# Optimization experiments

Measured on AMD Instinct MI355X. Metric: run time of the kernel, lower is better.

Reference implementation:

```python
import jax, jax.numpy as jnp
import numpy as np

B, N_HEADS, DIM, HS, WS = 8, 8, 256, 64, 64
CH = DIM // N_HEADS          # 32 head dim
HIDDEN = max(DIM // 2, 32)   # 128 SE hidden (r=2)
SCALE = CH ** -0.5
# CoaT-style CRPE: window sizes 3,5,7 over head groups (2,3,3)

def _dwconv(x, w, b):
    # depthwise conv, x: [B, Cg, H, W], w: [Cg, 1, kw, kw]
    y = jax.lax.conv_general_dilated(
        x, w, (1, 1), 'SAME',
        dimension_numbers=('NCHW', 'OIHW', 'NCHW'),
        feature_group_count=x.shape[1])
    return y + b[None, :, None, None]

def setup_inputs() -> dict:
    key = jax.random.key(0)
    ks = jax.random.split(key, 8)
    s = 0.02
    return {
        'x': jax.random.normal(ks[0], (B, HS * WS, DIM), jnp.float32),
        'qkv_w': jax.random.normal(ks[1], (3 * DIM, DIM), jnp.float32) * s,
        'qkv_b': jnp.zeros((3 * DIM,), jnp.float32),
        'proj_w': jax.random.normal(ks[2], (DIM, DIM), jnp.float32) * s,
        'proj_b': jnp.zeros((DIM,), jnp.float32),
        'se_w1': jax.random.normal(ks[3], (HIDDEN, DIM), jnp.float32) * s,
        'se_w2': jax.random.normal(ks[4], (N_HEADS, HIDDEN), jnp.float32) * s,
        'crpe_w3': jax.random.normal(ks[5], (2 * CH, 1, 3, 3), jnp.float32) * s,
        'crpe_b3': jnp.zeros((2 * CH,), jnp.float32),
        'crpe_w5': jax.random.normal(ks[6], (3 * CH, 1, 5, 5), jnp.float32) * s,
        'crpe_b5': jnp.zeros((3 * CH,), jnp.float32),
        'crpe_w7': jax.random.normal(ks[7], (3 * CH, 1, 7, 7), jnp.float32) * s,
        'crpe_b7': jnp.zeros((3 * CH,), jnp.float32),
        'H': HS, 'W': WS,
    }

def _crpe(q, v, H, W, w3, b3, w5, b5, w7, b7):
    # q, v: [B, h, N, Ch]; N == H*W
    Bq, h, N, Ch = q.shape
    v_img = v.transpose(0, 1, 3, 2).reshape(Bq, h * Ch, H, W)
    c0, c1 = 2 * Ch, 5 * Ch  # head splits (2,3,3)
    y = jnp.concatenate([
        _dwconv(v_img[:, :c0], w3, b3),
        _dwconv(v_img[:, c0:c1], w5, b5),
        _dwconv(v_img[:, c1:], w7, b7),
    ], axis=1)
    conv_v = y.reshape(Bq, h, Ch, N).transpose(0, 1, 3, 2)
    return q * conv_v  # Hadamard rel-pos term

def reference(x, qkv_w, qkv_b, proj_w, proj_b, se_w1, se_w2,
              crpe_w3, crpe_b3, crpe_w5, crpe_b5, crpe_w7, crpe_b7, H, W):
    Bx, N, C = x.shape
    qkv = (x @ qkv_w.T + qkv_b).reshape(Bx, N, 3, N_HEADS, CH)
    qkv = qkv.transpose(2, 0, 3, 1, 4)  # [3, B, h, N, Ch]
    q, k, v = qkv[0], qkv[1], qkv[2]
    crpe = _crpe(q, v, H, W, crpe_w3, crpe_b3, crpe_w5, crpe_b5, crpe_w7, crpe_b7)
    k_softmax = jax.nn.softmax(k, axis=2)  # softmax over tokens N
    ktv = jnp.einsum('bhnk,bhnv->bhkv', k_softmax, v)     # [B,h,Ch,Ch]
    factor_att = jnp.einsum('bhnk,bhkv->bhnv', q, ktv)    # [B,h,N,Ch]
    factor_att = SCALE * factor_att + crpe
    # SE-style domain gating: mean-pool over N -> conv1x1 -> relu -> conv1x1 -> sigmoid
    pooled = factor_att.mean(axis=2).reshape(Bx, N_HEADS * CH)  # [B, C]
    hid = jax.nn.relu(pooled @ se_w1.T)                         # [B, HIDDEN]
    gate = jax.nn.sigmoid(hid @ se_w2.T)                        # [B, h]
    out = factor_att * (1.0 + gate[:, :, None, None])           # gate*fa + fa
    out = out.transpose(0, 2, 1, 3).reshape(Bx, N, C)
    return out @ proj_w.T + proj_b
```

## Files before the change

kernel.cpp:

```cpp
#include <hip/hip_runtime.h>

namespace {

constexpr float kScale = 0.17677669529663687f;

typedef __attribute__((ext_vector_type(8))) short bf16x8;
typedef __attribute__((ext_vector_type(4))) short bf16x4;
typedef __attribute__((ext_vector_type(4))) float f32x4;

__device__ __forceinline__ short bf_hi(float x) {
  unsigned u = __float_as_uint(x);
  return (short)((u + 0x7FFFu + ((u >> 16) & 1u)) >> 16);
}
__device__ __forceinline__ short bf_lo(float x) {
  unsigned u = __float_as_uint(x);
  unsigned hi = (u + 0x7FFFu + ((u >> 16) & 1u)) & 0xFFFF0000u;
  float r = x - __uint_as_float(hi);
  unsigned u2 = __float_as_uint(r);
  return (short)((u2 + 0x7FFFu + ((u2 >> 16) & 1u)) >> 16);
}

__device__ __forceinline__ bf16x8 cvt8v(const float4 f0, const float4 f1,
                                        bool lo) {
  bf16x8 v;
  if (lo) {
    v[0] = bf_lo(f0.x); v[1] = bf_lo(f0.y); v[2] = bf_lo(f0.z);
    v[3] = bf_lo(f0.w); v[4] = bf_lo(f1.x); v[5] = bf_lo(f1.y);
    v[6] = bf_lo(f1.z); v[7] = bf_lo(f1.w);
  } else {
    v[0] = bf_hi(f0.x); v[1] = bf_hi(f0.y); v[2] = bf_hi(f0.z);
    v[3] = bf_hi(f0.w); v[4] = bf_hi(f1.x); v[5] = bf_hi(f1.y);
    v[6] = bf_hi(f1.z); v[7] = bf_hi(f1.w);
  }
  return v;
}

__global__ __launch_bounds__(1024) void wsplit2_kernel(
    const float* __restrict__ w, short* __restrict__ wsplit2) {
  const int nc = blockIdx.x;
  const int ct = nc / 24, j = nc % 24;
  const int r = j >> 3, kc = j & 7;
  const bool lo = (r == 1);
  const int u = threadIdx.x;
  const int col = u >> 2, kq = u & 3;
  const float* src = &w[(size_t)(ct * 256 + col) * 256 + kc * 32 + kq * 8];
  const float4 f0 = *reinterpret_cast<const float4*>(src);
  const float4 f1 = *reinterpret_cast<const float4*>(src + 4);
  *reinterpret_cast<bf16x8*>(&wsplit2[(size_t)nc * 8192 + u * 8]) =
      cvt8v(f0, f1, lo);
}

__global__ __launch_bounds__(1024) void pwsplit_kernel(
    const float* __restrict__ w, short* __restrict__ pw) {
  const int nc = blockIdx.x;
  const int r = nc >> 3, kc = nc & 7;
  const bool lo = (r == 1);
  const int u = threadIdx.x;
  const int col = u >> 2, kq = u & 3;
  const float* src = &w[(size_t)col * 256 + kc * 32 + kq * 8];
  const float4 f0 = *reinterpret_cast<const float4*>(src);
  const float4 f1 = *reinterpret_cast<const float4*>(src + 4);
  *reinterpret_cast<bf16x8*>(&pw[(size_t)nc * 8192 + u * 8]) =
      cvt8v(f0, f1, lo);
}

__global__ __launch_bounds__(512, 1) void qkv_mfma_kernel(
    const float* __restrict__ x, const short* __restrict__ wsplit2,
    const float* __restrict__ bias, float* __restrict__ q,
    float* __restrict__ kk, float* __restrict__ v) {
  __shared__ short As[128][520];
  __shared__ short Bs[256][40];
  const int tid = threadIdx.x;
  const int row0 = blockIdx.x * 128;
  const int wave = tid >> 6, lane = tid & 63;
  const int wr = (wave >> 2) * 64;
  const int wc = (wave & 3) * 64;
  const int l15 = lane & 15, l4 = lane >> 4;

  bf16x8 brgA[2], brgB[2];
  auto bload = [&](int nc, bf16x8 (&brg)[2]) {
    const short* src = wsplit2 + (size_t)nc * 8192;
#pragma unroll
    for (int i = 0; i < 2; ++i)
      brg[i] = *reinterpret_cast<const bf16x8*>(src + (tid + i * 512) * 8);
  };
  bload(0, brgA);
  bload(1, brgB);

#pragma unroll 4
  for (int i = 0; i < 16; ++i) {
    const int f = tid + i * 512;
    const int r = f >> 6, c = (f & 63) * 4;
    const float4 a4 = *reinterpret_cast<const float4*>(
        &x[(size_t)(row0 + r) * 256 + c]);
    bf16x4 h, l;
    h[0] = bf_hi(a4.x); h[1] = bf_hi(a4.y); h[2] = bf_hi(a4.z);
    h[3] = bf_hi(a4.w);
    l[0] = bf_lo(a4.x); l[1] = bf_lo(a4.y); l[2] = bf_lo(a4.z);
    l[3] = bf_lo(a4.w);
    *reinterpret_cast<bf16x4*>(&As[r][c]) = h;
    *reinterpret_cast<bf16x4*>(&As[r][256 + c]) = l;
  }
  __syncthreads();

  f32x4 acc[4][4];
  auto step = [&](int nc, bf16x8 (&brg)[2]) {
#pragma unroll
    for (int i = 0; i < 2; ++i) {
      const int u = tid + i * 512;
      *reinterpret_cast<bf16x8*>(&Bs[u >> 2][(u & 3) * 8]) = brg[i];
    }
    __syncthreads();
    if (nc + 2 < 72) bload(nc + 2, brg);
    const int j = nc % 24;
    const int r = j >> 3, kc = j & 7;
    const int aoff = (r == 2 ? 256 : 0) + kc * 32;
    bf16x8 af[4], bfr[4];
#pragma unroll
    for (int f = 0; f < 4; ++f) {
      af[f] = *reinterpret_cast<const bf16x8*>(
          &As[wr + f * 16 + l15][aoff + l4 * 8]);
      bfr[f] = *reinterpret_cast<const bf16x8*>(&Bs[wc + f * 16 + l15][l4 * 8]);
    }
#pragma unroll
    for (int fi = 0; fi < 4; ++fi)
#pragma unroll
      for (int fj = 0; fj < 4; ++fj)
        acc[fi][fj] = __builtin_amdgcn_mfma_f32_16x16x32_bf16(
            af[fi], bfr[fj], acc[fi][fj], 0, 0, 0);
    __syncthreads();
  };

  for (int ct = 0; ct < 3; ++ct) {
#pragma unroll
    for (int i = 0; i < 4; ++i)
#pragma unroll
      for (int j = 0; j < 4; ++j) acc[i][j] = (f32x4){0.f, 0.f, 0.f, 0.f};

    for (int j2 = 0; j2 < 12; ++j2) {
      step(ct * 24 + j2 * 2, brgA);
      step(ct * 24 + j2 * 2 + 1, brgB);
    }
    float* dst = (ct == 0) ? q : (ct == 1) ? kk : v;
#pragma unroll
    for (int fj = 0; fj < 4; ++fj) {
      const int col = wc + fj * 16 + l15;
      const int hh = col >> 5, cc = col & 31;
      const float bv = bias[ct * 256 + col];
#pragma unroll
      for (int fi = 0; fi < 4; ++fi) {
#pragma unroll
        for (int jj = 0; jj < 4; ++jj) {
          const int rr = row0 + wr + fi * 16 + l4 * 4 + jj;
          const int bb = rr >> 12, n = rr & 4095;
          dst[((size_t)(bb * 8 + hh) * 4096 + n) * 32 + cc] =
              acc[fi][fj][jj] + bv;
        }
      }
    }
  }
}

__global__ __launch_bounds__(256) void ktv_partial_kernel(
    const float* __restrict__ k, const float* __restrict__ v,
    float* __restrict__ pev, float* __restrict__ pe) {
  const int bh = blockIdx.x;
  const int chunk = blockIdx.y;
  const float* kb = k + (size_t)bh * 131072 + (size_t)chunk * 256 * 32;
  const float* vb = v + (size_t)bh * 131072 + (size_t)chunk * 256 * 32;
  __shared__ __align__(16) float ks[32][32];
  __shared__ __align__(16) float vs[32][32];
  const int t = threadIdx.x;
  const int kc = t >> 3;
  const int vg = (t & 7) * 4;
  const int sr = t >> 3, sc = (t & 7) * 4;
  float a0 = 0.f, a1 = 0.f, a2 = 0.f, a3 = 0.f, se = 0.f;
  for (int n0 = 0; n0 < 256; n0 += 32) {
    __syncthreads();
    const float4 k4 =
        *reinterpret_cast<const float4*>(&kb[(size_t)(n0 + sr) * 32 + sc]);
    const float4 v4 =
        *reinterpret_cast<const float4*>(&vb[(size_t)(n0 + sr) * 32 + sc]);
    *reinterpret_cast<float4*>(&ks[sr][sc]) = k4;
    *reinterpret_cast<float4*>(&vs[sr][sc]) = v4;
    __syncthreads();
#pragma unroll
    for (int r = 0; r < 32; ++r) {
      const float e = __expf(ks[r][kc]);
      se += e;
      const float4 vv = *reinterpret_cast<const float4*>(&vs[r][vg]);
      a0 = fmaf(e, vv.x, a0); a1 = fmaf(e, vv.y, a1);
      a2 = fmaf(e, vv.z, a2); a3 = fmaf(e, vv.w, a3);
    }
  }
  float* o = pev + ((size_t)(bh * 16 + chunk)) * 1024 + kc * 32 + vg;
  o[0] = a0; o[1] = a1; o[2] = a2; o[3] = a3;
  if ((t & 7) == 0) pe[(bh * 16 + chunk) * 32 + kc] = se;
}

__global__ __launch_bounds__(256) void ktv_reduce_kernel(
    const float* __restrict__ pev, const float* __restrict__ pe,
    float* __restrict__ ktv) {
  const int bh = blockIdx.x;
  const int t = threadIdx.x;
  const int kc = t >> 3, vg = (t & 7) * 4;
  float a0 = 0.f, a1 = 0.f, a2 = 0.f, a3 = 0.f, se = 0.f;
  for (int ch = 0; ch < 16; ++ch) {
    const float4 p4 = *reinterpret_cast<const float4*>(
        &pev[((size_t)(bh * 16 + ch)) * 1024 + kc * 32 + vg]);
    a0 += p4.x; a1 += p4.y; a2 += p4.z; a3 += p4.w;
    se += pe[(bh * 16 + ch) * 32 + kc];
  }
  const float inv = 1.0f / se;
  float* o = ktv + (size_t)bh * 1024 + kc * 32 + vg;
  o[0] = a0 * inv; o[1] = a1 * inv; o[2] = a2 * inv; o[3] = a3 * inv;
}

template <int K>
__device__ __forceinline__ void crpe_tile(const float (*lds)[64][32],
                                          const float* __restrict__ wch,
                                          float bias, int c, int x0,
                                          float* __restrict__ outbase) {
  constexpr int P = K / 2;
  constexpr int W = 8 + K - 1;
  float wreg[K * K];
#pragma unroll
  for (int i = 0; i < K * K; ++i) wreg[i] = wch[i];
#pragma unroll
  for (int yy = 0; yy < 4; ++yy) {
    float acc[8];
#pragma unroll
    for (int i = 0; i < 8; ++i) acc[i] = bias;
#pragma unroll
    for (int ky = 0; ky < K; ++ky) {
      const int lrow = yy + ky + (3 - P);
      float win[W];
#pragma unroll
      for (int j = 0; j < W; ++j) {
        const int xx = x0 + j - P;
        const int xc = min(max(xx, 0), 63);
        const float val = lds[lrow][xc][c];
        win[j] = (xx == xc) ? val : 0.f;
      }
#pragma unroll
      for (int kx = 0; kx < K; ++kx) {
        const float wgt = wreg[ky * K + kx];
#pragma unroll
        for (int i = 0; i < 8; ++i) acc[i] = fmaf(win[i + kx], wgt, acc[i]);
      }
    }
#pragma unroll
    for (int i = 0; i < 8; ++i)
      outbase[(size_t)(yy * 64 + x0 + i) * 32 + c] = acc[i];
  }
}

__global__ __launch_bounds__(256) void crpe_conv_kernel(
    const float* __restrict__ v, const float* __restrict__ w3,
    const float* __restrict__ b3, const float* __restrict__ w5,
    const float* __restrict__ b5, const float* __restrict__ w7,
    const float* __restrict__ b7, float* __restrict__ convv) {
  __shared__ __align__(16) float lds[10][64][32];
  const int t = threadIdx.x;
  const int y0 = blockIdx.x * 4;
  const int h = blockIdx.y, b = blockIdx.z;
  const float* vb = v + (size_t)(b * 8 + h) * 131072;
  const int ytop = y0 - 3;
  float4* lds4 = reinterpret_cast<float4*>(&lds[0][0][0]);
#pragma unroll
  for (int i = 0; i < 20; ++i) {
    const int idx = t + i * 256;
    const int row = idx >> 9;
    const int y = ytop + row;
    float4 val = {0.f, 0.f, 0.f, 0.f};
    if (y >= 0 && y < 64)
      val = *reinterpret_cast<const float4*>(
          &vb[(size_t)y * 2048 + (size_t)(idx & 511) * 4]);
    lds4[idx] = val;
  }
  __syncthreads();
  const int c = t & 31;
  const int x0 = (t >> 5) * 8;
  const int ch = h * 32 + c;
  float* outbase = convv + ((size_t)(b * 8 + h) * 4096 + y0 * 64) * 32;
  if (h < 2)
    crpe_tile<3>(lds, w3 + ch * 9, b3[ch], c, x0, outbase);
  else if (h < 5)
    crpe_tile<5>(lds, w5 + (ch - 64) * 25, b5[ch - 64], c, x0, outbase);
  else
    crpe_tile<7>(lds, w7 + (ch - 160) * 49, b7[ch - 160], c, x0, outbase);
}

__global__ __launch_bounds__(256) void factor_att_kernel(
    const float* __restrict__ q, const float* __restrict__ convv,
    const float* __restrict__ ktv, float* __restrict__ fa,
    float* __restrict__ partial) {
  const int b = blockIdx.z, h = blockIdx.y;
  const int n0 = blockIdx.x * 64;
  __shared__ __align__(16) float kt[32][32];
  __shared__ float qs[8][32];
  __shared__ float ps[8][32];
  const int t = threadIdx.x;
#pragma unroll
  for (int i = 0; i < 4; ++i) {
    const int idx = t + i * 256;
    kt[idx >> 5][idx & 31] = ktv[(size_t)(b * 8 + h) * 1024 + idx];
  }
  const size_t off = ((size_t)(b * 8 + h) * 4096 + n0) * 32;
  const float* qb = q + off;
  const float* cb = convv + off;
  float* fb = fa + off;
  const int c = t & 31, rs = t >> 5;
  float pool = 0.f;
  for (int i = 0; i < 8; ++i) {
    __syncthreads();
    qs[rs][c] = qb[i * 256 + t];
    __syncthreads();
    float s = 0.f;
#pragma unroll
    for (int kc = 0; kc < 32; ++kc) s = fmaf(qs[rs][kc], kt[kc][c], s);
    const float val = kScale * s + qs[rs][c] * cb[i * 256 + t];
    fb[i * 256 + t] = val;
    pool += val;
  }
  __syncthreads();
  ps[rs][c] = pool;
  __syncthreads();
  if (t < 32) {
    float s = 0.f;
#pragma unroll
    for (int r = 0; r < 8; ++r) s += ps[r][t];
    partial[((size_t)(b * 8 + h) * 64 + blockIdx.x) * 32 + t] = s;
  }
}

__global__ __launch_bounds__(256) void se_kernel(
    const float* __restrict__ partial, const float* __restrict__ w1,
    const float* __restrict__ w2, float* __restrict__ gfac) {
  const int b = blockIdx.x, t = threadIdx.x;
  __shared__ float pm[256];
  __shared__ float hid[128];
  {
    const int h = t >> 5, c = t & 31;
    const float* p = partial + ((size_t)(b * 8 + h) * 64) * 32 + c;
    float s = 0.f;
#pragma unroll 8
    for (int nc = 0; nc < 64; ++nc) s += p[nc * 32];
    pm[t] = s * (1.0f / 4096.0f);
  }
  __syncthreads();
  if (t < 128) {
    float s = 0.f;
    for (int ch = 0; ch < 256; ++ch) s = fmaf(pm[ch], w1[t * 256 + ch], s);
    hid[t] = fmaxf(s, 0.f);
  }
  __syncthreads();
  if (t < 8) {
    float g = 0.f;
    for (int j = 0; j < 128; ++j) g = fmaf(hid[j], w2[t * 128 + j], g);
    gfac[b * 8 + t] = 1.0f + 1.0f / (1.0f + __expf(-g));
  }
}

__global__ __launch_bounds__(512, 1) void proj_mfma_kernel(
    const float* __restrict__ fa, const float* __restrict__ gfac,
    const short* __restrict__ pwsplit, const float* __restrict__ bias,
    float* __restrict__ out) {
  __shared__ short As[128][520];
  __shared__ short Bs[256][40];
  const int tid = threadIdx.x;
  const int row0 = blockIdx.x * 128;
  const int wave = tid >> 6, lane = tid & 63;
  const int wr = (wave >> 2) * 64;
  const int wc = (wave & 3) * 64;
  const int l15 = lane & 15, l4 = lane >> 4;
  const int b = row0 >> 12;

  bf16x8 brgA[2], brgB[2];
  auto bload = [&](int nc, bf16x8 (&brg)[2]) {
    const short* src = pwsplit + (size_t)nc * 8192;
#pragma unroll
    for (int i = 0; i < 2; ++i)
      brg[i] = *reinterpret_cast<const bf16x8*>(src + (tid + i * 512) * 8);
  };
  bload(0, brgA);
  bload(1, brgB);

#pragma unroll 4
  for (int i = 0; i < 16; ++i) {
    const int f = tid + i * 512;
    const int r = f >> 6, c = (f & 63) * 4;
    const int hh = c >> 5, cc = c & 31;
    const int n = (row0 & 4095) + r;
    const float g = gfac[b * 8 + hh];
    float4 a4 = *reinterpret_cast<const float4*>(
        &fa[((size_t)(b * 8 + hh) * 4096 + n) * 32 + cc]);
    a4.x *= g; a4.y *= g; a4.z *= g; a4.w *= g;
    bf16x4 h, l;
    h[0] = bf_hi(a4.x); h[1] = bf_hi(a4.y); h[2] = bf_hi(a4.z);
    h[3] = bf_hi(a4.w);
    l[0] = bf_lo(a4.x); l[1] = bf_lo(a4.y); l[2] = bf_lo(a4.z);
    l[3] = bf_lo(a4.w);
    *reinterpret_cast<bf16x4*>(&As[r][c]) = h;
    *reinterpret_cast<bf16x4*>(&As[r][256 + c]) = l;
  }
  __syncthreads();

  f32x4 acc[4][4];
#pragma unroll
  for (int i = 0; i < 4; ++i)
#pragma unroll
    for (int j = 0; j < 4; ++j) acc[i][j] = (f32x4){0.f, 0.f, 0.f, 0.f};

  auto step = [&](int nc, bf16x8 (&brg)[2]) {
#pragma unroll
    for (int i = 0; i < 2; ++i) {
      const int u = tid + i * 512;
      *reinterpret_cast<bf16x8*>(&Bs[u >> 2][(u & 3) * 8]) = brg[i];
    }
    __syncthreads();
    if (nc + 2 < 24) bload(nc + 2, brg);
    const int r = nc >> 3, kc = nc & 7;
    const int aoff = (r == 2 ? 256 : 0) + kc * 32;
    bf16x8 af[4], bfr[4];
#pragma unroll
    for (int f = 0; f < 4; ++f) {
      af[f] = *reinterpret_cast<const bf16x8*>(
          &As[wr + f * 16 + l15][aoff + l4 * 8]);
      bfr[f] = *reinterpret_cast<const bf16x8*>(&Bs[wc + f * 16 + l15][l4 * 8]);
    }
#pragma unroll
    for (int fi = 0; fi < 4; ++fi)
#pragma unroll
      for (int fj = 0; fj < 4; ++fj)
        acc[fi][fj] = __builtin_amdgcn_mfma_f32_16x16x32_bf16(
            af[fi], bfr[fj], acc[fi][fj], 0, 0, 0);
    __syncthreads();
  };

  for (int j2 = 0; j2 < 12; ++j2) {
    step(j2 * 2, brgA);
    step(j2 * 2 + 1, brgB);
  }
#pragma unroll
  for (int fj = 0; fj < 4; ++fj) {
    const int col = wc + fj * 16 + l15;
    const float bv = bias[col];
#pragma unroll
    for (int fi = 0; fi < 4; ++fi) {
#pragma unroll
      for (int jj = 0; jj < 4; ++jj) {
        const int rr = row0 + wr + fi * 16 + l4 * 4 + jj;
        out[(size_t)rr * 256 + col] = acc[fi][fj][jj] + bv;
      }
    }
  }
}

}

extern "C" void kernel_launch(void* const* d_in, const int* in_sizes, int n_in,
                              void* d_out, int out_size, void* d_ws,
                              size_t ws_size, hipStream_t stream) {
  const float* x      = (const float*)d_in[0];
  const float* qkv_w  = (const float*)d_in[1];
  const float* qkv_b  = (const float*)d_in[2];
  const float* proj_w = (const float*)d_in[3];
  const float* proj_b = (const float*)d_in[4];
  const float* se_w1  = (const float*)d_in[5];
  const float* se_w2  = (const float*)d_in[6];
  const float* w3 = (const float*)d_in[7];
  const float* b3 = (const float*)d_in[8];
  const float* w5 = (const float*)d_in[9];
  const float* b5 = (const float*)d_in[10];
  const float* w7 = (const float*)d_in[11];
  const float* b7 = (const float*)d_in[12];
  float* out = (float*)d_out;
  float* ws = (float*)d_ws;

  const size_t SZ = (size_t)8 * 8 * 4096 * 32;
  float* q       = ws;
  float* kbuf    = ws + SZ;
  float* vbuf    = ws + 2 * SZ;
  float* ktv     = ws + 3 * SZ;
  float* kmaxp   = ktv + 65536;
  float* partial = kmaxp + 16384;
  float* gfac    = partial + 131072;
  float* pev = out;
  float* pe  = out + 64 * 16 * 1024;
  short* wsplit2 = (short*)(out + 2 * 1024 * 1024);
  short* pwsplit = (short*)q;
  (void)ws_size; (void)in_sizes; (void)n_in; (void)out_size;

  wsplit2_kernel<<<72, 1024, 0, stream>>>(qkv_w, wsplit2);
  qkv_mfma_kernel<<<256, 512, 0, stream>>>(x, wsplit2, qkv_b, q, kbuf, vbuf);
  ktv_partial_kernel<<<dim3(64, 16), 256, 0, stream>>>(kbuf, vbuf, pev, pe);
  ktv_reduce_kernel<<<64, 256, 0, stream>>>(pev, pe, ktv);
  crpe_conv_kernel<<<dim3(16, 8, 8), 256, 0, stream>>>(vbuf, w3, b3, w5, b5,
                                                       w7, b7, kbuf);
  factor_att_kernel<<<dim3(64, 8, 8), 256, 0, stream>>>(q, kbuf, ktv, vbuf,
                                                        partial);
  se_kernel<<<8, 256, 0, stream>>>(partial, se_w1, se_w2, gfac);
  pwsplit_kernel<<<24, 1024, 0, stream>>>(proj_w, pwsplit);
  proj_mfma_kernel<<<256, 512, 0, stream>>>(vbuf, gfac, pwsplit, proj_b, out);
}
```

Measured before the change: 180.5 us.

## Load weight fragments directly from global into registers, dropping LDS staging and barriers

In both the QKV and projection GEMM kernels, the B (weight) operand is no longer staged through shared memory. Each wave now loads its own MFMA B fragments straight from the pre-split global weight buffer, double-buffered one step ahead. This removes the LDS writes, LDS reads and the two __syncthreads per k-step. The cost is that each weight fragment is fetched redundantly by the two wave rows, putting more traffic on L2 and L1, and prefetch depth drops from two steps to one.

```diff
diff --git a/kernel.cpp b/kernel.cpp
--- a/kernel.cpp
+++ b/kernel.cpp
@@ -69,7 +69,6 @@
     const float* __restrict__ bias, float* __restrict__ q,
     float* __restrict__ kk, float* __restrict__ v) {
   __shared__ short As[128][520];
-  __shared__ short Bs[256][40];
   const int tid = threadIdx.x;
   const int row0 = blockIdx.x * 128;
   const int wave = tid >> 6, lane = tid & 63;
@@ -77,15 +76,15 @@
   const int wc = (wave & 3) * 64;
   const int l15 = lane & 15, l4 = lane >> 4;
 
-  bf16x8 brgA[2], brgB[2];
-  auto bload = [&](int nc, bf16x8 (&brg)[2]) {
-    const short* src = wsplit2 + (size_t)nc * 8192;
-#pragma unroll
-    for (int i = 0; i < 2; ++i)
-      brg[i] = *reinterpret_cast<const bf16x8*>(src + (tid + i * 512) * 8);
+  const short* bbase = wsplit2 + (size_t)(wc + l15) * 32 + l4 * 8;
+  bf16x8 bA[4], bB[4];
+  auto bload = [&](int nc, bf16x8 (&b)[4]) {
+#pragma unroll
+    for (int f = 0; f < 4; ++f)
+      b[f] = *reinterpret_cast<const bf16x8*>(bbase + (size_t)nc * 8192 +
+                                              f * 512);
   };
-  bload(0, brgA);
-  bload(1, brgB);
+  bload(0, bA);
 
 #pragma unroll 4
   for (int i = 0; i < 16; ++i) {
@@ -104,31 +103,22 @@
   __syncthreads();
 
   f32x4 acc[4][4];
-  auto step = [&](int nc, bf16x8 (&brg)[2]) {
-#pragma unroll
-    for (int i = 0; i < 2; ++i) {
-      const int u = tid + i * 512;
-      *reinterpret_cast<bf16x8*>(&Bs[u >> 2][(u & 3) * 8]) = brg[i];
-    }
-    __syncthreads();
-    if (nc + 2 < 72) bload(nc + 2, brg);
+  auto step = [&](int nc, bf16x8 (&use)[4], bf16x8 (&pf)[4]) {
+    if (nc + 1 < 72) bload(nc + 1, pf);
     const int j = nc % 24;
     const int r = j >> 3, kc = j & 7;
     const int aoff = (r == 2 ? 256 : 0) + kc * 32;
-    bf16x8 af[4], bfr[4];
-#pragma unroll
-    for (int f = 0; f < 4; ++f) {
+    bf16x8 af[4];
+#pragma unroll
+    for (int f = 0; f < 4; ++f)
       af[f] = *reinterpret_cast<const bf16x8*>(
           &As[wr + f * 16 + l15][aoff + l4 * 8]);
-      bfr[f] = *reinterpret_cast<const bf16x8*>(&Bs[wc + f * 16 + l15][l4 * 8]);
-    }
 #pragma unroll
     for (int fi = 0; fi < 4; ++fi)
 #pragma unroll
       for (int fj = 0; fj < 4; ++fj)
         acc[fi][fj] = __builtin_amdgcn_mfma_f32_16x16x32_bf16(
-            af[fi], bfr[fj], acc[fi][fj], 0, 0, 0);
-    __syncthreads();
+            af[fi], use[fj], acc[fi][fj], 0, 0, 0);
   };
 
   for (int ct = 0; ct < 3; ++ct) {
@@ -138,8 +128,8 @@
       for (int j = 0; j < 4; ++j) acc[i][j] = (f32x4){0.f, 0.f, 0.f, 0.f};
 
     for (int j2 = 0; j2 < 12; ++j2) {
-      step(ct * 24 + j2 * 2, brgA);
-      step(ct * 24 + j2 * 2 + 1, brgB);
+      step(ct * 24 + j2 * 2, bA, bB);
+      step(ct * 24 + j2 * 2 + 1, bB, bA);
     }
     float* dst = (ct == 0) ? q : (ct == 1) ? kk : v;
 #pragma unroll
@@ -367,7 +357,6 @@
     const short* __restrict__ pwsplit, const float* __restrict__ bias,
     float* __restrict__ out) {
   __shared__ short As[128][520];
-  __shared__ short Bs[256][40];
   const int tid = threadIdx.x;
   const int row0 = blockIdx.x * 128;
   const int wave = tid >> 6, lane = tid & 63;
@@ -376,15 +365,15 @@
   const int l15 = lane & 15, l4 = lane >> 4;
   const int b = row0 >> 12;
 
-  bf16x8 brgA[2], brgB[2];
-  auto bload = [&](int nc, bf16x8 (&brg)[2]) {
-    const short* src = pwsplit + (size_t)nc * 8192;
-#pragma unroll
-    for (int i = 0; i < 2; ++i)
-      brg[i] = *reinterpret_cast<const bf16x8*>(src + (tid + i * 512) * 8);
+  const short* bbase = pwsplit + (size_t)(wc + l15) * 32 + l4 * 8;
+  bf16x8 bA[4], bB[4];
+  auto bload = [&](int nc, bf16x8 (&bb)[4]) {
+#pragma unroll
+    for (int f = 0; f < 4; ++f)
+      bb[f] = *reinterpret_cast<const bf16x8*>(bbase + (size_t)nc * 8192 +
+                                               f * 512);
   };
-  bload(0, brgA);
-  bload(1, brgB);
+  bload(0, bA);
 
 #pragma unroll 4
   for (int i = 0; i < 16; ++i) {
@@ -412,35 +401,26 @@
 #pragma unroll
     for (int j = 0; j < 4; ++j) acc[i][j] = (f32x4){0.f, 0.f, 0.f, 0.f};
 
-  auto step = [&](int nc, bf16x8 (&brg)[2]) {
-#pragma unroll
-    for (int i = 0; i < 2; ++i) {
-      const int u = tid + i * 512;
-      *reinterpret_cast<bf16x8*>(&Bs[u >> 2][(u & 3) * 8]) = brg[i];
-    }
-    __syncthreads();
-    if (nc + 2 < 24) bload(nc + 2, brg);
+  auto step = [&](int nc, bf16x8 (&use)[4], bf16x8 (&pf)[4]) {
+    if (nc + 1 < 24) bload(nc + 1, pf);
     const int r = nc >> 3, kc = nc & 7;
     const int aoff = (r == 2 ? 256 : 0) + kc * 32;
-    bf16x8 af[4], bfr[4];
-#pragma unroll
-    for (int f = 0; f < 4; ++f) {
+    bf16x8 af[4];
+#pragma unroll
+    for (int f = 0; f < 4; ++f)
       af[f] = *reinterpret_cast<const bf16x8*>(
           &As[wr + f * 16 + l15][aoff + l4 * 8]);
-      bfr[f] = *reinterpret_cast<const bf16x8*>(&Bs[wc + f * 16 + l15][l4 * 8]);
-    }
 #pragma unroll
     for (int fi = 0; fi < 4; ++fi)
 #pragma unroll
       for (int fj = 0; fj < 4; ++fj)
         acc[fi][fj] = __builtin_amdgcn_mfma_f32_16x16x32_bf16(
-            af[fi], bfr[fj], acc[fi][fj], 0, 0, 0);
-    __syncthreads();
+            af[fi], use[fj], acc[fi][fj], 0, 0, 0);
   };
 
   for (int j2 = 0; j2 < 12; ++j2) {
-    step(j2 * 2, brgA);
-    step(j2 * 2 + 1, brgB);
+    step(j2 * 2, bA, bB);
+    step(j2 * 2 + 1, bB, bA);
   }
 #pragma unroll
   for (int fj = 0; fj < 4; ++fj) {
```

Result: faster. 175.4 us (-2.8%).
